# Kernel optimization log

Measured on AMD Instinct MI355X. Metric: run time of the kernel, lower is better.

Reference implementation:

```python
import jax, jax.numpy as jnp
import numpy as np

N, E = 10000, 30000
D_IN, E_DIM, H1, H2, C = 64, 16, 128, 64, 10


def setup_inputs() -> dict:
    key = jax.random.key(0)
    ks = jax.random.split(key, 12)
    x = jax.random.normal(ks[0], (N, D_IN), dtype=jnp.float32)
    edge_attr = jax.random.normal(ks[1], (E, E_DIM), dtype=jnp.float32)
    edge_index = jax.random.randint(ks[2], (2, E), 0, N, dtype=jnp.int64)
    # linear1: D_IN -> H1
    W1 = jax.random.normal(ks[3], (D_IN, H1), dtype=jnp.float32) / np.sqrt(D_IN)
    b1 = jnp.zeros((H1,), dtype=jnp.float32)
    # edge MLP 1: E_DIM -> H1*H2
    We1 = jax.random.normal(ks[4], (E_DIM, H1 * H2), dtype=jnp.float32) / np.sqrt(E_DIM)
    be1 = jnp.zeros((H1 * H2,), dtype=jnp.float32)
    root1 = jax.random.uniform(ks[5], (H1, H2), dtype=jnp.float32,
                               minval=-1.0 / np.sqrt(H1), maxval=1.0 / np.sqrt(H1))
    bias1 = jnp.zeros((H2,), dtype=jnp.float32)
    # edge MLP 2: E_DIM -> H2*C
    We2 = jax.random.normal(ks[6], (E_DIM, H2 * C), dtype=jnp.float32) / np.sqrt(E_DIM)
    be2 = jnp.zeros((H2 * C,), dtype=jnp.float32)
    root2 = jax.random.uniform(ks[7], (H2, C), dtype=jnp.float32,
                               minval=-1.0 / np.sqrt(H2), maxval=1.0 / np.sqrt(H2))
    bias2 = jnp.zeros((C,), dtype=jnp.float32)
    return {"x": x, "edge_attr": edge_attr, "edge_index": edge_index,
            "W1": W1, "b1": b1, "We1": We1, "be1": be1, "root1": root1, "bias1": bias1,
            "We2": We2, "be2": be2, "root2": root2, "bias2": bias2}


def _nnconv(h, src, dst, edge_attr, We, be, root, bias, c_in, c_out):
    # per-edge weight matrix from edge MLP: [E, c_in, c_out]
    W_e = (edge_attr @ We + be).reshape(-1, c_in, c_out)
    msg = jnp.einsum('ei,eio->eo', h[src], W_e)          # gather + batched matmul
    agg = jax.ops.segment_sum(msg, dst, num_segments=N)   # scatter-add to target nodes
    return agg + h @ root + bias


def reference(x, edge_attr, edge_index, W1, b1, We1, be1, root1, bias1,
              We2, be2, root2, bias2):
    src, dst = edge_index[0], edge_index[1]  # PyG: x_j = x[src], aggregate at dst
    h = jax.nn.relu(x @ W1 + b1)                               # [N, H1]
    h = jax.nn.relu(_nnconv(h, src, dst, edge_attr, We1, be1, root1, bias1, H1, H2))
    z = _nnconv(h, src, dst, edge_attr, We2, be2, root2, bias2, H2, C)
    return jax.nn.log_softmax(z, axis=1)
```

## Files before the change

kernel.cpp:

```cpp
#include <hip/hip_runtime.h>

#define N_NODES 10000
#define N_EDGES 30000
#define DIN     64
#define EDIM    16
#define H1      128
#define H2      64
#define C_OUT   10

typedef __bf16 bfrag __attribute__((ext_vector_type(8)));
typedef float  f32x4 __attribute__((ext_vector_type(4)));
typedef ushort ushort8 __attribute__((ext_vector_type(8)));

__device__ __forceinline__ ushort f2bf(float f) {
    union { float f; unsigned u; } x; x.f = f;
    unsigned r = x.u + 0x7fffu + ((x.u >> 16) & 1u);
    return (ushort)(r >> 16);
}
__device__ __forceinline__ float bf2f(ushort s) {
    union { unsigned u; float f; } x; x.u = ((unsigned)s) << 16;
    return x.f;
}

#define KA_B1   313
#define KA_B2   (KA_B1 + 576)
#define KA_B3   (KA_B2 + 48)
__global__ __launch_bounds__(256) void kA_prep(
        const float* __restrict__ x, const float* __restrict__ W1,
        const float* __restrict__ b1,
        const float* __restrict__ We1, const float* __restrict__ root1,
        const float* __restrict__ be1,
        const float* __restrict__ We2, const float* __restrict__ be2,
        const float* __restrict__ root2,
        ushort* __restrict__ h_bf, ushort* __restrict__ B1t,
        ushort* __restrict__ B2t) {
    int t = threadIdx.x;
    int bx = blockIdx.x;
    if (bx < KA_B1) {
        __shared__ float w_lds[DIN * H1];
        __shared__ float b_lds[H1];
        __shared__ float x_lds[8][DIN];
        for (int idx = t; idx < DIN * H1 / 4; idx += 256)
            ((float4*)w_lds)[idx] = ((const float4*)W1)[idx];
        if (t < H1) b_lds[t] = b1[t];
        #pragma unroll
        for (int sub = 0; sub < 4; ++sub) {
            int n0 = bx * 32 + sub * 8;
            if (t < 128) {
                int row = t >> 4, c4 = t & 15;
                int n = n0 + row;
                float4 v = make_float4(0.f, 0.f, 0.f, 0.f);
                if (n < N_NODES) v = ((const float4*)(x + (size_t)n * DIN))[c4];
                ((float4*)(x_lds[row]))[c4] = v;
            }
            __syncthreads();
            int nl = t >> 5;
            int o  = (t & 31) * 4;
            int n  = n0 + nl;
            float4 acc = *(const float4*)&b_lds[o];
            #pragma unroll 8
            for (int i = 0; i < DIN; ++i) {
                float xv = x_lds[nl][i];
                float4 w = *(const float4*)&w_lds[i * H1 + o];
                acc.x = fmaf(xv, w.x, acc.x);
                acc.y = fmaf(xv, w.y, acc.y);
                acc.z = fmaf(xv, w.z, acc.z);
                acc.w = fmaf(xv, w.w, acc.w);
            }
            if (n < N_NODES) {
                ushort4 s;
                s.x = f2bf(fmaxf(acc.x, 0.f));
                s.y = f2bf(fmaxf(acc.y, 0.f));
                s.z = f2bf(fmaxf(acc.z, 0.f));
                s.w = f2bf(fmaxf(acc.w, 0.f));
                *(ushort4*)&h_bf[(size_t)n * H1 + o] = s;
            }
            __syncthreads();
        }
    } else if (bx < KA_B2) {
        int idx = (bx - KA_B1) * 256 + t;
        int c = idx >> 7, i = idx & 127;
        float v;
        if (c < 1024) {
            int o = c >> 4, k = c & 15;
            v = We1[(size_t)k * (H1 * H2) + i * 64 + o];
        } else if (c < 1088) v = root1[i * 64 + (c - 1024)];
        else                 v = be1[i * 64 + (c - 1088)];
        B1t[idx] = f2bf(v);
    } else {
        int idx = (bx - KA_B2) * 256 + t;
        int c = idx >> 6, j = idx & 63;
        float v = 0.f;
        if (c < 160) {
            int cc = c >> 4, k = c & 15;
            v = We2[(size_t)k * 640 + j * 10 + cc];
        }
        else if (c < 170) v = be2[j * 10 + (c - 160)];
        else if (c < 180) v = root2[j * 10 + (c - 170)];
        B2t[idx] = f2bf(v);
    }
}

__global__ __launch_bounds__(256) void k3_mfma(
        const ushort* __restrict__ h_bf, const ushort* __restrict__ Bt,
        const float* __restrict__ bias1,
        ushort* __restrict__ G1t, float* __restrict__ agg1,
        float* __restrict__ hb1) {
    int t = threadIdx.x;
    int wave = t >> 6, lane = t & 63;
    int quad = lane >> 4, lrow = lane & 15;
    int yy = blockIdx.y;
    int mx = blockIdx.x;
    int nbase = mx * 128 + wave * 32;
    int ar0 = nbase + lrow;       if (ar0 > N_NODES - 1) ar0 = N_NODES - 1;
    int ar1 = nbase + 16 + lrow;  if (ar1 > N_NODES - 1) ar1 = N_NODES - 1;
    bfrag A0[4], A1[4];
    #pragma unroll
    for (int kc4 = 0; kc4 < 4; ++kc4) {
        A0[kc4] = *reinterpret_cast<const bfrag*>(
            h_bf + (size_t)ar0 * 128 + kc4 * 32 + quad * 8);
        A1[kc4] = *reinterpret_cast<const bfrag*>(
            h_bf + (size_t)ar1 * 128 + kc4 * 32 + quad * 8);
    }
    #pragma unroll
    for (int hy = 0; hy < 3; ++hy) {
        int y = yy * 3 + hy;
        const ushort* bbase = Bt + (size_t)y * 64 * 128;
        f32x4 acc0[4] = {}, acc1[4] = {};
        #pragma unroll
        for (int kc4 = 0; kc4 < 4; ++kc4) {
            #pragma unroll
            for (int ct = 0; ct < 4; ++ct) {
                bfrag b = *reinterpret_cast<const bfrag*>(
                    bbase + (size_t)(ct * 16 + lrow) * 128 + kc4 * 32 + quad * 8);
                acc0[ct] = __builtin_amdgcn_mfma_f32_16x16x32_bf16(A0[kc4], b, acc0[ct], 0, 0, 0);
                acc1[ct] = __builtin_amdgcn_mfma_f32_16x16x32_bf16(A1[kc4], b, acc1[ct], 0, 0, 0);
            }
        }
        #pragma unroll
        for (int half = 0; half < 2; ++half) {
            int rbase = nbase + half * 16 + quad * 4;
            #pragma unroll
            for (int ct = 0; ct < 4; ++ct) {
                int col = ct * 16 + lrow;
                f32x4 a = half ? acc1[ct] : acc0[ct];
                #pragma unroll
                for (int r = 0; r < 4; ++r) {
                    int n = rbase + r;
                    if (n >= N_NODES) continue;
                    float v = a[r];
                    if (y < 16) {
                        G1t[(size_t)n * 1024 + y * 64 + col] = f2bf(v);
                    } else if (y == 16) {
                        agg1[(size_t)n * 64 + col] = v + bias1[col];
                    } else {
                        hb1[(size_t)n * 64 + col] = v;
                    }
                }
            }
        }
    }
}

__global__ __launch_bounds__(256) void k4_edge1(
        const float* __restrict__ ea, const int* __restrict__ src_idx,
        const int* __restrict__ dst_idx, const ushort* __restrict__ G1t,
        const float* __restrict__ hb1, float* __restrict__ agg1) {
    int t = threadIdx.x;
    int e0 = blockIdx.x * 8 + (t >> 6) * 2;
    int o = t & 63;
    int s0 = src_idx[e0],     d0 = dst_idx[e0];
    int s1 = src_idx[e0 + 1], d1 = dst_idx[e0 + 1];
    const ushort* g0p = G1t + (size_t)s0 * 1024 + o * 16;
    const ushort* g1p = G1t + (size_t)s1 * 1024 + o * 16;
    ushort8 ga0 = *reinterpret_cast<const ushort8*>(g0p);
    ushort8 ga1 = *reinterpret_cast<const ushort8*>(g0p + 8);
    ushort8 gb0 = *reinterpret_cast<const ushort8*>(g1p);
    ushort8 gb1 = *reinterpret_cast<const ushort8*>(g1p + 8);
    float m0 = hb1[(size_t)s0 * 64 + o];
    float m1 = hb1[(size_t)s1 * 64 + o];
    const float* a0 = ea + (size_t)e0 * 16;
    const float* a1 = a0 + 16;
    #pragma unroll
    for (int k = 0; k < 8; ++k) {
        m0 = fmaf(a0[k], bf2f(ga0[k]), m0);
        m1 = fmaf(a1[k], bf2f(gb0[k]), m1);
    }
    #pragma unroll
    for (int k = 0; k < 8; ++k) {
        m0 = fmaf(a0[k + 8], bf2f(ga1[k]), m0);
        m1 = fmaf(a1[k + 8], bf2f(gb1[k]), m1);
    }
    atomicAdd(&agg1[(size_t)d0 * 64 + o], m0);
    atomicAdd(&agg1[(size_t)d1 * 64 + o], m1);
}

__global__ __launch_bounds__(256) void k56_mfma(
        const float* __restrict__ agg1, const ushort* __restrict__ B2t,
        const float* __restrict__ bias2,
        ushort* __restrict__ G2t, float* __restrict__ hb2,
        float* __restrict__ agg2) {
    int t = threadIdx.x;
    int wave = t >> 6, lane = t & 63;
    int quad = lane >> 4, lrow = lane & 15;
    int n0 = blockIdx.x * 64 + wave * 16;
    int arow = n0 + lrow; if (arow > N_NODES - 1) arow = N_NODES - 1;
    bfrag A[2];
    #pragma unroll
    for (int kk = 0; kk < 2; ++kk) {
        size_t off = (size_t)arow * 64 + kk * 32 + quad * 8;
        f32x4 p0 = *(const f32x4*)(agg1 + off);
        f32x4 p1 = *(const f32x4*)(agg1 + off + 4);
        bfrag a;
        #pragma unroll
        for (int j = 0; j < 4; ++j) {
            a[j]     = (__bf16)fmaxf(p0[j], 0.f);
            a[j + 4] = (__bf16)fmaxf(p1[j], 0.f);
        }
        A[kk] = a;
    }
    #pragma unroll
    for (int y = 0; y < 3; ++y) {
        f32x4 acc[4] = {};
        #pragma unroll
        for (int kk = 0; kk < 2; ++kk) {
            #pragma unroll
            for (int ct = 0; ct < 4; ++ct) {
                bfrag b = *reinterpret_cast<const bfrag*>(
                    B2t + (size_t)(y * 64 + ct * 16 + lrow) * 64 + kk * 32 + quad * 8);
                acc[ct] = __builtin_amdgcn_mfma_f32_16x16x32_bf16(A[kk], b, acc[ct], 0, 0, 0);
            }
        }
        #pragma unroll
        for (int ct = 0; ct < 4; ++ct) {
            int cg = y * 64 + ct * 16 + lrow;
            #pragma unroll
            for (int r = 0; r < 4; ++r) {
                int n = n0 + quad * 4 + r;
                if (n >= N_NODES) continue;
                float v = acc[ct][r];
                if (cg < 160)      G2t[(size_t)n * 160 + cg] = f2bf(v);
                else if (cg < 170) hb2[(size_t)n * 10 + (cg - 160)] = v;
                else if (cg < 180) agg2[(size_t)n * 10 + (cg - 170)] = v + bias2[cg - 170];
            }
        }
    }
}

__global__ __launch_bounds__(256) void k7_edge2(
        const float* __restrict__ ea, const int* __restrict__ src_idx,
        const int* __restrict__ dst_idx, const ushort* __restrict__ G2t,
        const float* __restrict__ hb2, float* __restrict__ agg2) {
    int tid = blockIdx.x * 256 + threadIdx.x;
    if (tid >= N_EDGES * 10) return;
    int e = tid / 10, c = tid - e * 10;
    int s = src_idx[e], d = dst_idx[e];
    float m = hb2[(size_t)s * 10 + c];
    const ushort* g = G2t + (size_t)s * 160 + c * 16;
    ushort8 g0 = *reinterpret_cast<const ushort8*>(g);
    ushort8 g1 = *reinterpret_cast<const ushort8*>(g + 8);
    const float* a = ea + (size_t)e * 16;
    f32x4 a0 = *(const f32x4*)a,       a1 = *(const f32x4*)(a + 4);
    f32x4 a2 = *(const f32x4*)(a + 8), a3 = *(const f32x4*)(a + 12);
    #pragma unroll
    for (int k = 0; k < 4; ++k) {
        m = fmaf(a0[k], bf2f(g0[k]), m);
        m = fmaf(a1[k], bf2f(g0[k + 4]), m);
        m = fmaf(a2[k], bf2f(g1[k]), m);
        m = fmaf(a3[k], bf2f(g1[k + 4]), m);
    }
    atomicAdd(&agg2[(size_t)d * 10 + c], m);
}

__global__ void k8_logsoftmax(const float* __restrict__ agg2,
                              float* __restrict__ out) {
    int n = blockIdx.x * blockDim.x + threadIdx.x;
    if (n >= N_NODES) return;
    float z[10]; float m = -1e30f;
    #pragma unroll
    for (int c = 0; c < 10; ++c) {
        z[c] = agg2[(size_t)n * 10 + c];
        m = fmaxf(m, z[c]);
    }
    float s = 0.f;
    #pragma unroll
    for (int c = 0; c < 10; ++c) s += expf(z[c] - m);
    float ls = logf(s);
    #pragma unroll
    for (int c = 0; c < 10; ++c) out[(size_t)n * 10 + c] = z[c] - m - ls;
}

extern "C" void kernel_launch(void* const* d_in, const int* in_sizes, int n_in,
                              void* d_out, int out_size, void* d_ws, size_t ws_size,
                              hipStream_t stream) {
    const float* x     = (const float*)d_in[0];
    const float* ea    = (const float*)d_in[1];
    const int*   eidx  = (const int*)d_in[2];
    const float* W1    = (const float*)d_in[3];
    const float* b1    = (const float*)d_in[4];
    const float* We1   = (const float*)d_in[5];
    const float* be1   = (const float*)d_in[6];
    const float* root1 = (const float*)d_in[7];
    const float* bias1 = (const float*)d_in[8];
    const float* We2   = (const float*)d_in[9];
    const float* be2   = (const float*)d_in[10];
    const float* root2 = (const float*)d_in[11];
    const float* bias2 = (const float*)d_in[12];
    float* out = (float*)d_out;
    const int* src_idx = eidx;
    const int* dst_idx = eidx + N_EDGES;

    float* ws = (float*)d_ws;
    ushort* h_bf = (ushort*)ws;
    ushort* B1t  = (ushort*)(ws + 640000);
    ushort* B2t  = (ushort*)(ws + 713728);
    ushort* G1t  = (ushort*)(ws + 719872);
    float* hb1  = ws + 719872 + 5120000;
    float* agg1 = hb1  + 640000;
    float* agg2 = agg1 + 640000;
    ushort* G2t = (ushort*)(agg2 + 100000);
    float* hb2  = agg2 + 100000 + 800000;

    kA_prep<<<KA_B3, 256, 0, stream>>>(x, W1, b1, We1, root1, be1,
                                       We2, be2, root2, h_bf, B1t, B2t);
    k3_mfma<<<dim3(79, 6), 256, 0, stream>>>(h_bf, B1t, bias1, G1t, agg1, hb1);
    k4_edge1<<<3750, 256, 0, stream>>>(ea, src_idx, dst_idx, G1t, hb1, agg1);
    k56_mfma<<<157, 256, 0, stream>>>(agg1, B2t, bias2, G2t, hb2, agg2);
    k7_edge2<<<1172, 256, 0, stream>>>(ea, src_idx, dst_idx, G2t, hb2, agg2);
    k8_logsoftmax<<<40, 256, 0, stream>>>(agg2, out);
}
```

Measured before the change: 139.0 us.

## Fuse layer-1 node GEMM with edge messages via LDS and src-bucketed edges

Fuses the layer-1 per-node MFMA GEMM with the edge message computation. A single prep block buckets edges by source-node tile (CSR-style offsets), so each GEMM block can consume its G1/hb1 tile directly from LDS. This avoids writing and re-reading the large bf16 G1t and hb1 intermediates in global memory. In exchange, the root term is atomically accumulated, agg1 must be zeroed in prep, and the single-block bucketing pass is serial. The edge loop per block depends on per-tile edge counts and may be load-imbalanced.

Measured after the change: 272.2 us. 1.96x slower.

```diff
diff --git a/kernel.cpp b/kernel.cpp
--- a/kernel.cpp
+++ b/kernel.cpp
@@ -25,15 +25,18 @@
 #define KA_B1   313
 #define KA_B2   (KA_B1 + 576)
 #define KA_B3   (KA_B2 + 48)
+#define KA_B4   (KA_B3 + 40)
+#define KA_TOT  (KA_B4 + 1)
 __global__ __launch_bounds__(256) void kA_prep(
         const float* __restrict__ x, const float* __restrict__ W1,
         const float* __restrict__ b1,
         const float* __restrict__ We1, const float* __restrict__ root1,
         const float* __restrict__ be1,
         const float* __restrict__ We2, const float* __restrict__ be2,
-        const float* __restrict__ root2,
+        const float* __restrict__ root2, const int* __restrict__ src_idx,
         ushort* __restrict__ h_bf, ushort* __restrict__ B1t,
-        ushort* __restrict__ B2t) {
+        ushort* __restrict__ B2t, float* __restrict__ agg1,
+        int* __restrict__ row_ptr, int* __restrict__ ebuf) {
     int t = threadIdx.x;
     int bx = blockIdx.x;
     if (bx < KA_B1) {
@@ -87,7 +90,7 @@
         } else if (c < 1088) v = root1[i * 64 + (c - 1024)];
         else                 v = be1[i * 64 + (c - 1088)];
         B1t[idx] = f2bf(v);
-    } else {
+    } else if (bx < KA_B3) {
         int idx = (bx - KA_B2) * 256 + t;
         int c = idx >> 6, j = idx & 63;
         float v = 0.f;
@@ -98,20 +101,48 @@
         else if (c < 170) v = be2[j * 10 + (c - 160)];
         else if (c < 180) v = root2[j * 10 + (c - 170)];
         B2t[idx] = f2bf(v);
-    }
-}
-
-__global__ __launch_bounds__(256) void k3_mfma(
+    } else if (bx < KA_B4) {
+        float4 z = make_float4(0.f, 0.f, 0.f, 0.f);
+        for (int i = (bx - KA_B3) * 256 + t; i < 160000; i += 40 * 256)
+            ((float4*)agg1)[i] = z;
+    } else {
+        __shared__ int cnt[80];
+        __shared__ int ofs[80];
+        for (int i = t; i < 80; i += 256) cnt[i] = 0;
+        __syncthreads();
+        for (int e = t; e < N_EDGES; e += 256)
+            atomicAdd(&cnt[src_idx[e] >> 7], 1);
+        __syncthreads();
+        if (t == 0) {
+            int s = 0;
+            for (int b = 0; b < 79; ++b) {
+                ofs[b] = s; row_ptr[b] = s; s += cnt[b];
+            }
+            row_ptr[79] = s;
+        }
+        __syncthreads();
+        for (int e = t; e < N_EDGES; e += 256) {
+            int p = atomicAdd(&ofs[src_idx[e] >> 7], 1);
+            ebuf[p] = e;
+        }
+    }
+}
+
+__global__ __launch_bounds__(256) void k34_mfma_edge(
         const ushort* __restrict__ h_bf, const ushort* __restrict__ Bt,
-        const float* __restrict__ bias1,
-        ushort* __restrict__ G1t, float* __restrict__ agg1,
-        float* __restrict__ hb1) {
+        const float* __restrict__ bias1, const float* __restrict__ ea,
+        const int* __restrict__ src_idx, const int* __restrict__ dst_idx,
+        const int* __restrict__ row_ptr, const int* __restrict__ ebuf,
+        float* __restrict__ agg1) {
+    __shared__ ushort lds_G[128][200];
+    __shared__ float  lds_hb[128][17];
     int t = threadIdx.x;
     int wave = t >> 6, lane = t & 63;
     int quad = lane >> 4, lrow = lane & 15;
     int yy = blockIdx.y;
     int mx = blockIdx.x;
-    int nbase = mx * 128 + wave * 32;
+    int nblk = mx * 128;
+    int nbase = nblk + wave * 32;
     int ar0 = nbase + lrow;       if (ar0 > N_NODES - 1) ar0 = N_NODES - 1;
     int ar1 = nbase + 16 + lrow;  if (ar1 > N_NODES - 1) ar1 = N_NODES - 1;
     bfrag A0[4], A1[4];
@@ -122,8 +153,8 @@
         A1[kc4] = *reinterpret_cast<const bfrag*>(
             h_bf + (size_t)ar1 * 128 + kc4 * 32 + quad * 8);
     }
-    #pragma unroll
-    for (int hy = 0; hy < 3; ++hy) {
+    int ylim = (yy == 5) ? 2 : 3;
+    for (int hy = 0; hy < ylim; ++hy) {
         int y = yy * 3 + hy;
         const ushort* bbase = Bt + (size_t)y * 64 * 128;
         f32x4 acc0[4] = {}, acc1[4] = {};
@@ -139,60 +170,71 @@
         }
         #pragma unroll
         for (int half = 0; half < 2; ++half) {
-            int rbase = nbase + half * 16 + quad * 4;
+            int lbase = wave * 32 + half * 16 + quad * 4;
             #pragma unroll
             for (int ct = 0; ct < 4; ++ct) {
                 int col = ct * 16 + lrow;
                 f32x4 a = half ? acc1[ct] : acc0[ct];
                 #pragma unroll
                 for (int r = 0; r < 4; ++r) {
-                    int n = rbase + r;
-                    if (n >= N_NODES) continue;
                     float v = a[r];
                     if (y < 16) {
-                        G1t[(size_t)n * 1024 + y * 64 + col] = f2bf(v);
-                    } else if (y == 16) {
-                        agg1[(size_t)n * 64 + col] = v + bias1[col];
+                        lds_G[lbase + r][hy * 64 + col] = f2bf(v);
                     } else {
-                        hb1[(size_t)n * 64 + col] = v;
+                        int n = nblk + lbase + r;
+                        if (n < N_NODES)
+                            atomicAdd(&agg1[(size_t)n * 64 + col], v + bias1[col]);
                     }
                 }
             }
         }
     }
-}
-
-__global__ __launch_bounds__(256) void k4_edge1(
-        const float* __restrict__ ea, const int* __restrict__ src_idx,
-        const int* __restrict__ dst_idx, const ushort* __restrict__ G1t,
-        const float* __restrict__ hb1, float* __restrict__ agg1) {
-    int t = threadIdx.x;
-    int e0 = blockIdx.x * 8 + (t >> 6) * 2;
-    int o = t & 63;
-    int s0 = src_idx[e0],     d0 = dst_idx[e0];
-    int s1 = src_idx[e0 + 1], d1 = dst_idx[e0 + 1];
-    const ushort* g0p = G1t + (size_t)s0 * 1024 + o * 16;
-    const ushort* g1p = G1t + (size_t)s1 * 1024 + o * 16;
-    ushort8 ga0 = *reinterpret_cast<const ushort8*>(g0p);
-    ushort8 ga1 = *reinterpret_cast<const ushort8*>(g0p + 8);
-    ushort8 gb0 = *reinterpret_cast<const ushort8*>(g1p);
-    ushort8 gb1 = *reinterpret_cast<const ushort8*>(g1p + 8);
-    float m0 = hb1[(size_t)s0 * 64 + o];
-    float m1 = hb1[(size_t)s1 * 64 + o];
-    const float* a0 = ea + (size_t)e0 * 16;
-    const float* a1 = a0 + 16;
-    #pragma unroll
-    for (int k = 0; k < 8; ++k) {
-        m0 = fmaf(a0[k], bf2f(ga0[k]), m0);
-        m1 = fmaf(a1[k], bf2f(gb0[k]), m1);
-    }
-    #pragma unroll
-    for (int k = 0; k < 8; ++k) {
-        m0 = fmaf(a0[k + 8], bf2f(ga1[k]), m0);
-        m1 = fmaf(a1[k + 8], bf2f(gb1[k]), m1);
-    }
-    atomicAdd(&agg1[(size_t)d0 * 64 + o], m0);
-    atomicAdd(&agg1[(size_t)d1 * 64 + o], m1);
+    {
+        int o0h = (yy == 5) ? 48 : 12 * yy;
+        const ushort* bb = Bt + (size_t)(1088 + o0h) * 128;
+        f32x4 h0 = {}, h1 = {};
+        #pragma unroll
+        for (int kc4 = 0; kc4 < 4; ++kc4) {
+            bfrag b = *reinterpret_cast<const bfrag*>(
+                bb + (size_t)lrow * 128 + kc4 * 32 + quad * 8);
+            h0 = __builtin_amdgcn_mfma_f32_16x16x32_bf16(A0[kc4], b, h0, 0, 0, 0);
+            h1 = __builtin_amdgcn_mfma_f32_16x16x32_bf16(A1[kc4], b, h1, 0, 0, 0);
+        }
+        #pragma unroll
+        for (int half = 0; half < 2; ++half) {
+            int lbase = wave * 32 + half * 16 + quad * 4;
+            f32x4 a = half ? h1 : h0;
+            #pragma unroll
+            for (int r = 0; r < 4; ++r)
+                lds_hb[lbase + r][lrow] = a[r];
+        }
+    }
+    __syncthreads();
+    int start = row_ptr[mx];
+    int cnt   = row_ptr[mx + 1] - start;
+    int W     = (yy == 5) ? 4 : 12;
+    int o0    = (yy == 5) ? 60 : 12 * yy;
+    int hboff = (yy == 5) ? 12 : 0;
+    for (int i = t; i < cnt; i += 256) {
+        int e = ebuf[start + i];
+        int s = src_idx[e], d = dst_idx[e];
+        int sl = s - nblk;
+        const f32x4* ap = reinterpret_cast<const f32x4*>(ea + (size_t)e * 16);
+        f32x4 a0 = ap[0], a1 = ap[1], a2 = ap[2], a3 = ap[3];
+        for (int ol = 0; ol < W; ++ol) {
+            ushort8 g0 = *reinterpret_cast<const ushort8*>(&lds_G[sl][ol * 16]);
+            ushort8 g1 = *reinterpret_cast<const ushort8*>(&lds_G[sl][ol * 16 + 8]);
+            float m = lds_hb[sl][ol + hboff];
+            #pragma unroll
+            for (int k = 0; k < 4; ++k) {
+                m = fmaf(a0[k], bf2f(g0[k]), m);
+                m = fmaf(a1[k], bf2f(g0[k + 4]), m);
+                m = fmaf(a2[k], bf2f(g1[k]), m);
+                m = fmaf(a3[k], bf2f(g1[k + 4]), m);
+            }
+            atomicAdd(&agg1[(size_t)d * 64 + o0 + ol], m);
+        }
+    }
 }
 
 __global__ __launch_bounds__(256) void k56_mfma(
@@ -314,17 +356,19 @@
     ushort* h_bf = (ushort*)ws;
     ushort* B1t  = (ushort*)(ws + 640000);
     ushort* B2t  = (ushort*)(ws + 713728);
-    ushort* G1t  = (ushort*)(ws + 719872);
-    float* hb1  = ws + 719872 + 5120000;
-    float* agg1 = hb1  + 640000;
+    int* ebuf    = (int*)(ws + 719872);
+    int* row_ptr = (int*)(ws + 749888);
+    float* agg1 = ws + 749984;
     float* agg2 = agg1 + 640000;
     ushort* G2t = (ushort*)(agg2 + 100000);
     float* hb2  = agg2 + 100000 + 800000;
 
-    kA_prep<<<KA_B3, 256, 0, stream>>>(x, W1, b1, We1, root1, be1,
-                                       We2, be2, root2, h_bf, B1t, B2t);
-    k3_mfma<<<dim3(79, 6), 256, 0, stream>>>(h_bf, B1t, bias1, G1t, agg1, hb1);
-    k4_edge1<<<3750, 256, 0, stream>>>(ea, src_idx, dst_idx, G1t, hb1, agg1);
+    kA_prep<<<KA_TOT, 256, 0, stream>>>(x, W1, b1, We1, root1, be1,
+                                        We2, be2, root2, src_idx,
+                                        h_bf, B1t, B2t, agg1, row_ptr, ebuf);
+    k34_mfma_edge<<<dim3(79, 6), 256, 0, stream>>>(h_bf, B1t, bias1, ea,
+                                                   src_idx, dst_idx,
+                                                   row_ptr, ebuf, agg1);
     k56_mfma<<<157, 256, 0, stream>>>(agg1, B2t, bias2, G2t, hb2, agg2);
     k7_edge2<<<1172, 256, 0, stream>>>(ea, src_idx, dst_idx, G2t, hb2, agg2);
     k8_logsoftmax<<<40, 256, 0, stream>>>(agg2, out);
```
